# Performance work log

Hardware: AMD Instinct MI355X
Metric: run time of the kernel (lower is better)

The kernel has to match this reference:

```python
import jax, jax.numpy as jnp
import numpy as np

NUM_HEADS = 16
HEAD_DIM = 64  # latent_dim // num_heads = 1024 // 16


def setup_inputs() -> dict:
    key = jax.random.key(0)
    k1, k2, k3, k4 = jax.random.split(key, 4)
    B, S, C = 4, 2048, 1024
    x = jax.random.normal(k1, (B, S, C), dtype=jnp.float32)
    # torch nn.Linear weight layout: [out_features, in_features]
    W_qkv = jax.random.normal(k2, (2 * 1024 + C, C), dtype=jnp.float32) * (C ** -0.5)
    W_out = jax.random.normal(k3, (C, C), dtype=jnp.float32) * (C ** -0.5)
    b_out = jax.random.normal(k4, (C,), dtype=jnp.float32) * 0.01
    return {"x": x, "W_qkv": W_qkv, "W_out": W_out, "b_out": b_out}


def reference(x, W_qkv, W_out, b_out):
    B, S, C = x.shape
    H, CH = NUM_HEADS, HEAD_DIM
    qkv = jnp.einsum('bsc,oc->bso', x, W_qkv)          # [B, S, 2*latent + C]
    qkv = qkv.reshape(B, S, H, -1)                      # per-head: [CH, CH, C//H]
    q = qkv[..., :CH]
    k = qkv[..., CH:2 * CH]
    v = qkv[..., 2 * CH:]
    energy = jnp.einsum('bqhc,bkhc->bhqk', q, k)        # full score matrix
    scale = jnp.asarray(C, x.dtype) ** 0.5              # note: original scales by sqrt(C), not sqrt(head_dim)
    attn = jax.nn.softmax(energy / scale, axis=-1)
    out = jnp.einsum('bhqk,bkhc->bqhc', attn, v).reshape(B, S, -1)
    out = jnp.einsum('bsc,oc->bso', out, W_out) + b_out
    return out + x
```

## Files before the change

### kernel.cpp

```cpp
#include <hip/hip_runtime.h>
#include <hip/hip_bf16.h>
#include <stdint.h>

#define BB 4
#define SS 2048
#define CC 1024
#define HH 16
#define DD 64
#define MTOT (BB*SS)
#define NQKV 3072

typedef __attribute__((ext_vector_type(8))) short short8;
typedef __attribute__((ext_vector_type(4))) float f32x4;

#define MFMA16(A,B,C) __builtin_amdgcn_mfma_f32_16x16x32_bf16((A),(B),(C),0,0,0)
#define BARRIER() asm volatile("s_barrier" ::: "memory")

__device__ __forceinline__ ushort f2bf(float f) {
  uint32_t u = __builtin_bit_cast(uint32_t, f);
  u += 0x7FFFu + ((u >> 16) & 1u);
  return (ushort)(u >> 16);
}

__device__ __forceinline__ unsigned cvtpk(float lo, float hi) {
  unsigned r;
  asm("v_cvt_pk_bf16_f32 %0, %1, %2" : "=v"(r) : "v"(lo), "v"(hi));
  return r;
}

__device__ __forceinline__ float hw_exp2(float x) {
  float r;
  asm("v_exp_f32 %0, %1" : "=v"(r) : "v"(x));
  return r;
}

__global__ void cvt_kernel(const float* __restrict__ src, ushort* __restrict__ dst, int n4) {
  int stride = gridDim.x * blockDim.x;
  for (int i = blockIdx.x * blockDim.x + threadIdx.x; i < n4; i += stride) {
    float4 v = reinterpret_cast<const float4*>(src)[i];
    ushort4 o;
    o.x = f2bf(v.x); o.y = f2bf(v.y); o.z = f2bf(v.z); o.w = f2bf(v.w);
    reinterpret_cast<ushort4*>(dst)[i] = o;
  }
}

__device__ __forceinline__ void stage_half128(const ushort* __restrict__ gsrc, ushort* ldsbase, int tid) {
  #pragma unroll
  for (int ld = 0; ld < 4; ++ld) {
    int ci = ld * 256 + tid;
    int row = ci >> 3, slot = ci & 7;
    const ushort* src = gsrc + (size_t)row * 1024 + ((slot ^ (row & 7)) << 3);
    __builtin_amdgcn_global_load_lds(
        (const __attribute__((address_space(1))) uint32_t*)src,
        (__attribute__((address_space(3))) uint32_t*)(ldsbase + ci * 8), 16, 0, 0);
  }
}

__device__ __forceinline__ short8 rd_frag(const ushort* Lb, int row, int slot) {
  return *(const short8*)(Lb + row * 64 + ((slot ^ (row & 7)) << 3));
}

__device__ __forceinline__ void core128(const ushort* __restrict__ A, const ushort* __restrict__ Bw,
                                        int m0, int n0, ushort* L, f32x4 acc[4][4]) {
  const int tid = threadIdx.x, lane = tid & 63, w = tid >> 6;
  const int q = lane & 15, g = lane >> 4;
  const int wm = (w >> 1) * 64, wn = (w & 1) * 64;
  const ushort* Ag = A + (size_t)m0 * 1024;
  const ushort* Bg = Bw + (size_t)n0 * 1024;

  #pragma unroll
  for (int tt = 0; tt < 2; ++tt) {
    stage_half128(Ag + tt * 64, L + tt * 16384, tid);
    stage_half128(Bg + tt * 64, L + tt * 16384 + 8192, tid);
  }
  asm volatile("s_waitcnt vmcnt(8)" ::: "memory");
  BARRIER();

  #pragma unroll 1
  for (int t = 0; t < 16; ++t) {
    const ushort* La = L + (t & 1) * 16384;
    const ushort* Lb = La + 8192;
    short8 af[4][2], bf[4][2];
    #pragma unroll
    for (int mi = 0; mi < 4; ++mi)
      #pragma unroll
      for (int ks = 0; ks < 2; ++ks)
        af[mi][ks] = rd_frag(La, wm + mi * 16 + q, ks * 4 + g);
    #pragma unroll
    for (int nj = 0; nj < 4; ++nj)
      #pragma unroll
      for (int ks = 0; ks < 2; ++ks)
        bf[nj][ks] = rd_frag(Lb, wn + nj * 16 + q, ks * 4 + g);
    #pragma unroll
    for (int mi = 0; mi < 4; ++mi)
      #pragma unroll
      for (int nj = 0; nj < 4; ++nj) {
        acc[mi][nj] = MFMA16(af[mi][0], bf[nj][0], acc[mi][nj]);
        acc[mi][nj] = MFMA16(af[mi][1], bf[nj][1], acc[mi][nj]);
      }
    BARRIER();
    if (t <= 13) {
      ushort* Ls = L + (t & 1) * 16384;
      stage_half128(Ag + (t + 2) * 64, Ls, tid);
      stage_half128(Bg + (t + 2) * 64, Ls + 8192, tid);
      asm volatile("s_waitcnt vmcnt(8)" ::: "memory");
      BARRIER();
    } else if (t == 14) {
      asm volatile("s_waitcnt vmcnt(0)" ::: "memory");
      BARRIER();
    }
  }
}

__global__ __launch_bounds__(256, 2) void gemm_qkv(const ushort* __restrict__ xb, const ushort* __restrict__ wqkv,
                                                   ushort* __restrict__ qfbuf, ushort* __restrict__ kfbuf,
                                                   ushort* __restrict__ vfbuf) {
  __shared__ __align__(16) ushort L[32768];
  const int bid = blockIdx.x;
  const int xcd = bid & 7, r = bid >> 3;
  const int m0 = (r / 3) * 128, n0 = (xcd * 3 + (r % 3)) * 128;

  f32x4 acc[4][4];
  #pragma unroll
  for (int i = 0; i < 4; ++i)
    #pragma unroll
    for (int j = 0; j < 4; ++j) acc[i][j] = f32x4{0.f, 0.f, 0.f, 0.f};
  core128(xb, wqkv, m0, n0, L, acc);

  const int lane = threadIdx.x & 63, wave = threadIdx.x >> 6;
  const int g = lane >> 4, q = lane & 15;
  const int wm = (wave >> 1) * 64, wn = (wave & 1) * 64;
  #pragma unroll
  for (int j = 0; j < 4; ++j) {
    int n = n0 + wn + j * 16 + q;
    int h = n / 192;
    int rem = n - h * 192;
    int which = rem >> 6;
    int c = rem & 63;
    float scl = (which == 0) ? 0.045084222f : 1.0f;
    #pragma unroll
    for (int i = 0; i < 4; ++i) {
      int mb = m0 + wm + i * 16 + g * 4;
      #pragma unroll
      for (int rr = 0; rr < 4; ++rr) {
        int m = mb + rr;
        int b = m >> 11, s = m & 2047;
        int bh = b * 16 + h;
        ushort val = f2bf(acc[i][j][rr] * scl);
        if (which < 2) {
          int jt = s >> 4, c0 = c >> 5, lane2 = ((c >> 3) & 3) * 16 + (s & 15), e = c & 7;
          size_t idx = ((((size_t)bh * 128 + jt) * 2 + c0) * 64 + lane2) * 8 + e;
          if (which == 0) qfbuf[idx] = val; else kfbuf[idx] = val;
        } else {
          int jc = s >> 5, gg = (s >> 3) & 3, e = s & 7, ct = c >> 4, qq = c & 15;
          size_t idx = ((((size_t)bh * 64 + jc) * 4 + ct) * 64 + gg * 16 + qq) * 8 + e;
          vfbuf[idx] = val;
        }
      }
    }
  }
}

__global__ __launch_bounds__(256, 2) void gemm_out(const ushort* __restrict__ ab, const ushort* __restrict__ wout,
                                                   const float* __restrict__ x, const float* __restrict__ bias,
                                                   float* __restrict__ out) {
  __shared__ __align__(16) ushort L[32768];
  const int bid = blockIdx.x;
  const int sw = (bid & 7) * 64 + (bid >> 3);
  const int m0 = (sw & 63) * 128, n0 = (sw >> 6) * 128;

  f32x4 acc[4][4];
  #pragma unroll
  for (int i = 0; i < 4; ++i)
    #pragma unroll
    for (int j = 0; j < 4; ++j) acc[i][j] = f32x4{0.f, 0.f, 0.f, 0.f};
  core128(ab, wout, m0, n0, L, acc);

  const int lane = threadIdx.x & 63, wave = threadIdx.x >> 6;
  const int g = lane >> 4, q = lane & 15;
  const int wm = (wave >> 1) * 64, wn = (wave & 1) * 64;
  #pragma unroll
  for (int j = 0; j < 4; ++j) {
    int n = n0 + wn + j * 16 + q;
    float bj = bias[n];
    #pragma unroll
    for (int i = 0; i < 4; ++i) {
      int mb = m0 + wm + i * 16 + g * 4;
      #pragma unroll
      for (int rr = 0; rr < 4; ++rr) {
        size_t m = (size_t)(mb + rr);
        out[m * CC + n] = acc[i][j][rr] + bj + x[m * CC + n];
      }
    }
  }
}

__device__ __forceinline__ void attn_step(const short8 kf[4][2], const short8 vf[2][4],
                                          const short8 qf[2][2], const short8 onesf,
                                          f32x4 oa[2][4], f32x4 la[2],
                                          ushort* pw0, int g, int q) {
  const f32x4 zed = {0.f, 0.f, 0.f, 0.f};
  #pragma unroll
  for (int t = 0; t < 2; ++t) {
    f32x4 sa[4];
    __builtin_amdgcn_s_setprio(1);
    #pragma unroll
    for (int jt = 0; jt < 4; ++jt) {
      sa[jt] = MFMA16(kf[jt][0], qf[t][0], zed);
      sa[jt] = MFMA16(kf[jt][1], qf[t][1], sa[jt]);
    }
    __builtin_amdgcn_s_setprio(0);
    ushort* pw = pw0 + t * 1152;
    #pragma unroll
    for (int jt = 0; jt < 4; ++jt) {
      uint2 wv;
      wv.x = cvtpk(hw_exp2(sa[jt][0]), hw_exp2(sa[jt][1]));
      wv.y = cvtpk(hw_exp2(sa[jt][2]), hw_exp2(sa[jt][3]));
      *reinterpret_cast<uint2*>(pw + q * 72 + jt * 16 + 4 * g) = wv;
    }
    #pragma unroll
    for (int jc = 0; jc < 2; ++jc) {
      short8 pa = *reinterpret_cast<const short8*>(pw + q * 72 + jc * 32 + g * 8);
      __builtin_amdgcn_s_setprio(1);
      #pragma unroll
      for (int ct = 0; ct < 4; ++ct)
        oa[t][ct] = MFMA16(pa, vf[jc][ct], oa[t][ct]);
      la[t] = MFMA16(pa, onesf, la[t]);
      __builtin_amdgcn_s_setprio(0);
    }
  }
}

__global__ __launch_bounds__(256) void attn_kernel(const ushort* __restrict__ QF, const ushort* __restrict__ KF,
                                                   const ushort* __restrict__ VF, ushort* __restrict__ aout) {
  __shared__ ushort Ps[4][2][16 * 72];
  const int bid = blockIdx.x;
  const int xcd = bid & 7, rr = bid >> 3;
  const int qb = rr & 15, bh = xcd + (rr >> 4) * 8;
  const int lane = threadIdx.x & 63, wave = threadIdx.x >> 6;
  const int g = lane >> 4, q = lane & 15;
  const int qt0 = (qb * 4 + wave) * 2;
  const f32x4 zed = {0.f, 0.f, 0.f, 0.f};

  const ushort* Qb = QF + (size_t)bh * 131072 + lane * 8;
  const ushort* Kp = KF + (size_t)bh * 131072 + lane * 8;
  const ushort* Vp = VF + (size_t)bh * 131072 + lane * 8;
  ushort* pw0 = Ps[wave][0];

  short8 onesf;
  #pragma unroll
  for (int e = 0; e < 8; ++e) onesf[e] = (short)0x3F80;

  short8 qf[2][2];
  #pragma unroll
  for (int t = 0; t < 2; ++t)
    #pragma unroll
    for (int c0 = 0; c0 < 2; ++c0)
      qf[t][c0] = *(const short8*)(Qb + ((size_t)(qt0 + t) * 2 + c0) * 512);

  f32x4 oa[2][4], la[2];
  #pragma unroll
  for (int t = 0; t < 2; ++t) {
    la[t] = zed;
    #pragma unroll
    for (int ct = 0; ct < 4; ++ct) oa[t][ct] = zed;
  }

  short8 kfA[4][2], kfB[4][2], vfA[2][4], vfB[2][4];
  #pragma unroll
  for (int jt = 0; jt < 4; ++jt)
    #pragma unroll
    for (int c0 = 0; c0 < 2; ++c0)
      kfA[jt][c0] = *(const short8*)(Kp + ((size_t)jt * 2 + c0) * 512);

  #pragma unroll 1
  for (int i = 0; i < 32; i += 2) {
    #pragma unroll
    for (int jc = 0; jc < 2; ++jc)
      #pragma unroll
      for (int ct = 0; ct < 4; ++ct)
        vfA[jc][ct] = *(const short8*)(Vp + ((size_t)jc * 4 + ct) * 512);
    #pragma unroll
    for (int jt = 0; jt < 4; ++jt)
      #pragma unroll
      for (int c0 = 0; c0 < 2; ++c0)
        kfB[jt][c0] = *(const short8*)(Kp + 4096 + ((size_t)jt * 2 + c0) * 512);

    attn_step(kfA, vfA, qf, onesf, oa, la, pw0, g, q);

    #pragma unroll
    for (int jc = 0; jc < 2; ++jc)
      #pragma unroll
      for (int ct = 0; ct < 4; ++ct)
        vfB[jc][ct] = *(const short8*)(Vp + 4096 + ((size_t)jc * 4 + ct) * 512);
    if (i + 2 < 32) {
      #pragma unroll
      for (int jt = 0; jt < 4; ++jt)
        #pragma unroll
        for (int c0 = 0; c0 < 2; ++c0)
          kfA[jt][c0] = *(const short8*)(Kp + 8192 + ((size_t)jt * 2 + c0) * 512);
    }

    attn_step(kfB, vfB, qf, onesf, oa, la, pw0, g, q);

    Kp += 8192; Vp += 8192;
  }

  const int b = bh >> 4, h = bh & 15;
  #pragma unroll
  for (int t = 0; t < 2; ++t) {
    float inv[4];
    #pragma unroll
    for (int r2 = 0; r2 < 4; ++r2) inv[r2] = 1.0f / la[t][r2];
    #pragma unroll
    for (int ct = 0; ct < 4; ++ct) {
      size_t rowb = (size_t)b * SS + (qt0 + t) * 16 + 4 * g;
      int col = h * DD + ct * 16 + q;
      aout[(rowb + 0) * CC + col] = f2bf(oa[t][ct][0] * inv[0]);
      aout[(rowb + 1) * CC + col] = f2bf(oa[t][ct][1] * inv[1]);
      aout[(rowb + 2) * CC + col] = f2bf(oa[t][ct][2] * inv[2]);
      aout[(rowb + 3) * CC + col] = f2bf(oa[t][ct][3] * inv[3]);
    }
  }
}

extern "C" void kernel_launch(void* const* d_in, const int* in_sizes, int n_in,
                              void* d_out, int out_size, void* d_ws, size_t ws_size,
                              hipStream_t stream) {
  const float* x    = (const float*)d_in[0];
  const float* wqkv = (const float*)d_in[1];
  const float* wout = (const float*)d_in[2];
  const float* bias = (const float*)d_in[3];
  float* out = (float*)d_out;

  ushort* xb    = (ushort*)d_ws;
  ushort* wqkvb = xb + (size_t)8 * 1024 * 1024;
  ushort* woutb = wqkvb + (size_t)3 * 1024 * 1024;
  ushort* qfbuf = woutb + (size_t)1024 * 1024;
  ushort* kfbuf = qfbuf + (size_t)8 * 1024 * 1024;
  ushort* vfbuf = kfbuf + (size_t)8 * 1024 * 1024;
  ushort* aout  = vfbuf + (size_t)8 * 1024 * 1024;

  hipLaunchKernelGGL(cvt_kernel, dim3(2048), dim3(256), 0, stream, x, xb, 8 * 1024 * 1024 / 4);
  hipLaunchKernelGGL(cvt_kernel, dim3(1536), dim3(256), 0, stream, wqkv, wqkvb, 3 * 1024 * 1024 / 4);
  hipLaunchKernelGGL(cvt_kernel, dim3(512), dim3(256), 0, stream, wout, woutb, 1024 * 1024 / 4);

  hipLaunchKernelGGL(gemm_qkv, dim3(1536), dim3(256), 0, stream,
                     xb, wqkvb, qfbuf, kfbuf, vfbuf);
  hipLaunchKernelGGL(attn_kernel, dim3(1024), dim3(256), 0, stream,
                     qfbuf, kfbuf, vfbuf, aout);
  hipLaunchKernelGGL(gemm_out, dim3(512), dim3(256), 0, stream,
                     aout, woutb, x, bias, out);
}
```

Baseline: 212.1 us.

## Stage QKV GEMM epilogue through LDS for vectorized stores; merge conversion kernels

The QKV GEMM epilogue now writes bf16 results into a swizzled LDS tile, synchronizes, and then emits 16-byte vectorized stores in the Q/K/V fragment layouts, replacing scattered 2-byte global stores. The three fp32-to-bf16 conversion launches are merged into one kernel that covers all three buffers, removing two launches. The LDS staging adds a barrier and extra LDS traffic, and the V path still gathers elements one at a time from LDS.

```diff
diff --git a/kernel.cpp b/kernel.cpp
--- a/kernel.cpp
+++ b/kernel.cpp
@@ -34,13 +34,20 @@
   return r;
 }
 
-__global__ void cvt_kernel(const float* __restrict__ src, ushort* __restrict__ dst, int n4) {
+__global__ void cvt3_kernel(const float* __restrict__ a, ushort* __restrict__ da, int na4,
+                            const float* __restrict__ b, ushort* __restrict__ db, int nb4,
+                            const float* __restrict__ c, ushort* __restrict__ dc, int nc4) {
+  int total = na4 + nb4 + nc4;
   int stride = gridDim.x * blockDim.x;
-  for (int i = blockIdx.x * blockDim.x + threadIdx.x; i < n4; i += stride) {
-    float4 v = reinterpret_cast<const float4*>(src)[i];
+  for (int i = blockIdx.x * blockDim.x + threadIdx.x; i < total; i += stride) {
+    const float4* s; ushort4* d; int k;
+    if (i < na4)            { s = (const float4*)a; d = (ushort4*)da; k = i; }
+    else if (i < na4 + nb4) { s = (const float4*)b; d = (ushort4*)db; k = i - na4; }
+    else                    { s = (const float4*)c; d = (ushort4*)dc; k = i - na4 - nb4; }
+    float4 v = s[k];
     ushort4 o;
     o.x = f2bf(v.x); o.y = f2bf(v.y); o.z = f2bf(v.z); o.w = f2bf(v.w);
-    reinterpret_cast<ushort4*>(dst)[i] = o;
+    d[k] = o;
   }
 }
 
@@ -117,8 +124,8 @@
                                                    ushort* __restrict__ vfbuf) {
   __shared__ __align__(16) ushort L[32768];
   const int bid = blockIdx.x;
-  const int xcd = bid & 7, r = bid >> 3;
-  const int m0 = (r / 3) * 128, n0 = (xcd * 3 + (r % 3)) * 128;
+  const int xcd = bid & 7, r0 = bid >> 3;
+  const int m0 = (r0 / 3) * 128, n0 = (xcd * 3 + (r0 % 3)) * 128;
 
   f32x4 acc[4][4];
   #pragma unroll
@@ -130,32 +137,56 @@
   const int lane = threadIdx.x & 63, wave = threadIdx.x >> 6;
   const int g = lane >> 4, q = lane & 15;
   const int wm = (wave >> 1) * 64, wn = (wave & 1) * 64;
+  const int s0 = m0 & 2047, bb = m0 >> 11;
+
   #pragma unroll
   for (int j = 0; j < 4; ++j) {
     int n = n0 + wn + j * 16 + q;
     int h = n / 192;
-    int rem = n - h * 192;
-    int which = rem >> 6;
-    int c = rem & 63;
+    int which = (n - h * 192) >> 6;
     float scl = (which == 0) ? 0.045084222f : 1.0f;
+    int nc = wn + j * 16 + q;
     #pragma unroll
     for (int i = 0; i < 4; ++i) {
-      int mb = m0 + wm + i * 16 + g * 4;
       #pragma unroll
       for (int rr = 0; rr < 4; ++rr) {
-        int m = mb + rr;
-        int b = m >> 11, s = m & 2047;
-        int bh = b * 16 + h;
-        ushort val = f2bf(acc[i][j][rr] * scl);
-        if (which < 2) {
-          int jt = s >> 4, c0 = c >> 5, lane2 = ((c >> 3) & 3) * 16 + (s & 15), e = c & 7;
-          size_t idx = ((((size_t)bh * 128 + jt) * 2 + c0) * 64 + lane2) * 8 + e;
-          if (which == 0) qfbuf[idx] = val; else kfbuf[idx] = val;
-        } else {
-          int jc = s >> 5, gg = (s >> 3) & 3, e = s & 7, ct = c >> 4, qq = c & 15;
-          size_t idx = ((((size_t)bh * 64 + jc) * 4 + ct) * 64 + gg * 16 + qq) * 8 + e;
-          vfbuf[idx] = val;
+        int mr = wm + i * 16 + g * 4 + rr;
+        L[mr * 128 + (nc ^ ((mr & 7) << 4))] = f2bf(acc[i][j][rr] * scl);
+      }
+    }
+  }
+  __syncthreads();
+
+  {
+    const int n_g = n0 + wave * 32;
+    const int h = n_g / 192, rem = n_g - h * 192, which = rem >> 6;
+    const int bh = bb * 16 + h;
+    if (which < 2) {
+      ushort* dst0 = (which == 0) ? qfbuf : kfbuf;
+      const int c0 = (rem & 63) >> 5;
+      #pragma unroll
+      for (int k = 0; k < 8; ++k) {
+        int jt = (s0 >> 4) + k;
+        int mr = k * 16 + (lane & 15);
+        int nc0 = wave * 32 + (lane >> 4) * 8;
+        short8 v = *(const short8*)(L + mr * 128 + (nc0 ^ ((mr & 7) << 4)));
+        *(short8*)(dst0 + ((((size_t)bh * 128 + jt) * 2 + c0) * 64 + lane) * 8) = v;
+      }
+    } else {
+      const int ct0 = (rem & 63) >> 4;
+      #pragma unroll
+      for (int k = 0; k < 8; ++k) {
+        int jcr = k >> 1, ct = ct0 + (k & 1);
+        int nc = wave * 32 + (k & 1) * 16 + (lane & 15);
+        int mrb = jcr * 32 + (lane >> 4) * 8;
+        short8 v;
+        #pragma unroll
+        for (int e = 0; e < 8; ++e) {
+          int mr = mrb + e;
+          v[e] = (short)L[mr * 128 + (nc ^ ((mr & 7) << 4))];
         }
+        int jc = (s0 >> 5) + jcr;
+        *(short8*)(vfbuf + ((((size_t)bh * 64 + jc) * 4 + ct) * 64 + lane) * 8) = v;
       }
     }
   }
@@ -341,9 +372,10 @@
   ushort* vfbuf = kfbuf + (size_t)8 * 1024 * 1024;
   ushort* aout  = vfbuf + (size_t)8 * 1024 * 1024;
 
-  hipLaunchKernelGGL(cvt_kernel, dim3(2048), dim3(256), 0, stream, x, xb, 8 * 1024 * 1024 / 4);
-  hipLaunchKernelGGL(cvt_kernel, dim3(1536), dim3(256), 0, stream, wqkv, wqkvb, 3 * 1024 * 1024 / 4);
-  hipLaunchKernelGGL(cvt_kernel, dim3(512), dim3(256), 0, stream, wout, woutb, 1024 * 1024 / 4);
+  hipLaunchKernelGGL(cvt3_kernel, dim3(2048), dim3(256), 0, stream,
+                     x, xb, 8 * 1024 * 1024 / 4,
+                     wqkv, wqkvb, 3 * 1024 * 1024 / 4,
+                     wout, woutb, 1024 * 1024 / 4);
 
   hipLaunchKernelGGL(gemm_qkv, dim3(1536), dim3(256), 0, stream,
                      xb, wqkvb, qfbuf, kfbuf, vfbuf);
```

Result: faster. 191.2 us (-9.9%).
